# Performance work log

Measured on AMD Instinct MI355X. Metric: run time of the kernel, lower is better.

## Reference

```python
import jax, jax.numpy as jnp
import numpy as np

B, L, S = 4, 512, 100
NG, GS = 19, 5          # 19 clades of 5 species; species 95..99 are singleton clades
VOCAB = 6
HID = 512
HPOOL = 4               # num_attention_heads // 2
D = 64                  # hidden_size / num_attention_heads
ALL = HPOOL * D         # 256
FIRE_H = 32
TIME_SCALE = 1.0        # from time_enc = 'fire_1'
MAX_DIST = 20.0         # config.max_evol_dist


def setup_inputs() -> dict:
    key = jax.random.key(0)
    ks = jax.random.split(key, 10)
    return {
        "source_ids": jax.random.randint(ks[0], (B, L, S), 0, VOCAB, dtype=jnp.int32),
        "in_clade_phylo_dist": jax.random.uniform(ks[1], (S,), dtype=jnp.float32) * MAX_DIST,
        "attn_w_emb": jax.random.normal(ks[2], (VOCAB, HPOOL), dtype=jnp.float32) * 0.02,
        "value_emb": jax.random.normal(ks[3], (VOCAB, ALL), dtype=jnp.float32) * 0.02,
        "ffn_w": jax.random.normal(ks[4], (ALL, HID), dtype=jnp.float32) * 0.02,
        "ffn_b": jnp.zeros((HID,), dtype=jnp.float32),
        "embed_tab": jax.random.normal(ks[5], (VOCAB, HID), dtype=jnp.float32) * 0.02,
        "fire_c": jnp.float32(100.0),
        "fire_w1": jax.random.normal(ks[6], (FIRE_H,), dtype=jnp.float32) * 0.5,
        "fire_w2": jax.random.normal(ks[7], (FIRE_H,), dtype=jnp.float32) * 0.5,
    }


def reference(source_ids, in_clade_phylo_dist, attn_w_emb, value_emb,
              ffn_w, ffn_b, embed_tab, fire_c, fire_w1, fire_w2):
    # --- FIRE time bias: scalar MLP per species distance -> bias[s] ---
    c = jnp.maximum(fire_c, 0.0)
    rel = in_clade_phylo_dist * TIME_SCALE                      # [S]
    rel = jnp.log(c * rel + 1.0) / jnp.log(c * MAX_DIST + 1.0)  # [S]
    h = jax.nn.silu(rel[:, None] * fire_w1[None, :])            # [S, FIRE_H]
    bias = h @ fire_w2                                          # [S]

    # --- multi-species clades: embedding-based attention pooling ---
    grp = jnp.arange(NG * GS).reshape(NG, GS)                   # static clade layout
    ids_g = source_ids[..., :NG * GS].reshape(B, L, NG, GS)     # [B,L,NG,GS]
    scores = jnp.swapaxes(attn_w_emb[ids_g], -1, -2)            # [B,L,NG,H,GS]
    scores = scores + bias[grp][None, None, :, None, :]
    probs = jax.nn.softmax(scores, axis=-1)                     # dropout p=0 (eval)
    vals = value_emb[ids_g].reshape(B, L, NG, GS, HPOOL, D)     # [B,L,NG,GS,H,D]
    pooled = jnp.einsum('blnhg,blnghd->blnhd', probs, vals)     # [B,L,NG,H,D]
    pooled = pooled.reshape(B, L, NG, ALL)
    pooled = pooled @ ffn_w + ffn_b                             # [B,L,NG,HID]

    # --- singleton clades: plain embedding lookup ---
    singles = embed_tab[source_ids[..., NG * GS:]]              # [B,L,5,HID]

    return jnp.concatenate([pooled, singles], axis=-2)          # [B,L,24,HID]
```

## Files before the change

kernel.cpp:

```cpp
#include <hip/hip_runtime.h>

#define B_      4
#define L_      512
#define S_      100
#define NG_     19
#define GS_     5
#define VOCAB_  6
#define HID_    512
#define HPOOL_  4
#define D_      64
#define ALL_    256
#define FIREH_  32
#define MAXDIST_ 20.0f


__global__ __launch_bounds__(128) void prep_kernel(
    const float* __restrict__ dist,
    const float* __restrict__ value_emb,
    const float* __restrict__ ffn_w,
    const float* __restrict__ fire_c,
    const float* __restrict__ fire_w1,
    const float* __restrict__ fire_w2,
    float* __restrict__ bias_out,
    float* __restrict__ W2_out)
{
  const int b = blockIdx.x;
  const int t = threadIdx.x;
  if (b < VOCAB_ * HPOOL_ * 4) {
    const int q   = b >> 2;
    const int col = (b & 3) * 128 + t;
    const int v = q >> 2;
    const int h = q & 3;
    float acc = 0.f;
#pragma unroll
    for (int k = 0; k < D_; ++k) {
      acc = fmaf(value_emb[v * ALL_ + h * D_ + k],
                 ffn_w[(h * D_ + k) * HID_ + col], acc);
    }
    W2_out[q * HID_ + col] = acc;
  } else {
    if (t < S_) {
      const float c = fmaxf(fire_c[0], 0.f);
      const float denom = logf(fmaf(c, MAXDIST_, 1.f));
      const float rel = logf(fmaf(c, dist[t], 1.f)) / denom;
      float acc = 0.f;
#pragma unroll
      for (int i = 0; i < FIREH_; ++i) {
        const float x = rel * fire_w1[i];
        const float s = x / (1.f + expf(-x));
        acc = fmaf(s, fire_w2[i], acc);
      }
      bias_out[t] = acc;
    }
  }
}

__global__ __launch_bounds__(256) void main_kernel(
    const int*   __restrict__ ids,
    const float* __restrict__ attn_w,
    const float* __restrict__ embed_tab,
    const float* __restrict__ ffn_b,
    const float* __restrict__ bias,
    const float* __restrict__ W2,
    float* __restrict__ out)
{
  const int bl = blockIdx.x;
  const int t  = threadIdx.x;

  __shared__ int s_ids[S_];
  __shared__ float s_bias[S_];
  __shared__ float s_aw[VOCAB_ * HPOOL_];
  __shared__ __align__(16) float s_cw[NG_][24];

  if (t < S_) s_ids[t] = ids[bl * S_ + t];
  else if (t >= 100 && t < 200) s_bias[t - 100] = bias[t - 100];
  else if (t >= 224 && t < 248) s_aw[t - 224] = attn_w[t - 224];
#pragma unroll
  for (int i = t; i < NG_ * 24; i += 256) ((float*)s_cw)[i] = 0.f;
  __syncthreads();

  if (t < NG_ * HPOOL_) {
    const int n = t >> 2;
    const int h = t & 3;
    int   idg[GS_];
    float p[GS_];
    float m = -1e30f;
#pragma unroll
    for (int g = 0; g < GS_; ++g) {
      idg[g] = s_ids[n * GS_ + g];
      p[g] = s_aw[idg[g] * HPOOL_ + h] + s_bias[n * GS_ + g];
      m = fmaxf(m, p[g]);
    }
    float s = 0.f;
#pragma unroll
    for (int g = 0; g < GS_; ++g) { p[g] = expf(p[g] - m); s += p[g]; }
    const float inv = 1.f / s;
#pragma unroll
    for (int g = 0; g < GS_; ++g) {
      s_cw[n][idg[g] * HPOOL_ + h] += p[g] * inv;
    }
  }
  __syncthreads();

  float2 w2r[24];
#pragma unroll
  for (int q = 0; q < 24; ++q)
    w2r[q] = *(const float2*)&W2[q * HID_ + 2 * t];
  const float2 bb = *(const float2*)&ffn_b[2 * t];

  float* op = out + (size_t)bl * 24 * HID_ + 2 * t;

  for (int n = 0; n < NG_; ++n) {
    float2 acc = bb;
    const float4* cw4 = (const float4*)s_cw[n];
#pragma unroll
    for (int q4 = 0; q4 < 6; ++q4) {
      const float4 c = cw4[q4];
      acc.x = fmaf(c.x, w2r[q4 * 4 + 0].x, acc.x);
      acc.y = fmaf(c.x, w2r[q4 * 4 + 0].y, acc.y);
      acc.x = fmaf(c.y, w2r[q4 * 4 + 1].x, acc.x);
      acc.y = fmaf(c.y, w2r[q4 * 4 + 1].y, acc.y);
      acc.x = fmaf(c.z, w2r[q4 * 4 + 2].x, acc.x);
      acc.y = fmaf(c.z, w2r[q4 * 4 + 2].y, acc.y);
      acc.x = fmaf(c.w, w2r[q4 * 4 + 3].x, acc.x);
      acc.y = fmaf(c.w, w2r[q4 * 4 + 3].y, acc.y);
    }
    *(float2*)(op + n * HID_) = acc;
  }

#pragma unroll
  for (int j = 0; j < 5; ++j) {
    const int id = s_ids[NG_ * GS_ + j];
    *(float2*)(op + (NG_ + j) * HID_) =
        *(const float2*)&embed_tab[id * HID_ + 2 * t];
  }
}

extern "C" void kernel_launch(void* const* d_in, const int* in_sizes, int n_in,
                              void* d_out, int out_size, void* d_ws, size_t ws_size,
                              hipStream_t stream) {
  const int*   src_ids = (const int*)  d_in[0];
  const float* dist    = (const float*)d_in[1];
  const float* attn_w  = (const float*)d_in[2];
  const float* valemb  = (const float*)d_in[3];
  const float* ffn_w   = (const float*)d_in[4];
  const float* ffn_b   = (const float*)d_in[5];
  const float* emb_tab = (const float*)d_in[6];
  const float* fire_c  = (const float*)d_in[7];
  const float* fire_w1 = (const float*)d_in[8];
  const float* fire_w2 = (const float*)d_in[9];

  float* out  = (float*)d_out;
  float* ws   = (float*)d_ws;
  float* bias = ws;
  float* W2   = ws + 128;

  hipLaunchKernelGGL(prep_kernel, dim3(97), dim3(128), 0, stream,
                     dist, valemb, ffn_w, fire_c, fire_w1, fire_w2, bias, W2);
  hipLaunchKernelGGL(main_kernel, dim3(B_ * L_), dim3(256), 0, stream,
                     src_ids, attn_w, emb_tab, ffn_b, bias, W2, out);
}
```

Baseline: 31.47 us.

## Process two positions per block, hoist W2 loads, use nontemporal stores

Each block now handles two (b,l) positions, which halves the grid and reuses the per-thread W2 register tile and bias across both positions. The W2 loads are moved before the first barrier so they overlap the shared-memory setup. Output writes use nontemporal stores to avoid cache pollution, and the singleton IDs are read directly from global memory. Fewer blocks may reduce parallelism on a large GPU, with 1024 blocks still available.

After: 32.33 us. +2.7%, slower.

```diff
diff --git a/kernel.cpp b/kernel.cpp
--- a/kernel.cpp
+++ b/kernel.cpp
@@ -12,6 +12,9 @@
 #define ALL_    256
 #define FIREH_  32
 #define MAXDIST_ 20.0f
+
+typedef float f32x2 __attribute__((ext_vector_type(2)));
+typedef float f32x4 __attribute__((ext_vector_type(4)));
 
 
 __global__ __launch_bounds__(128) void prep_kernel(
@@ -64,30 +67,40 @@
     const float* __restrict__ W2,
     float* __restrict__ out)
 {
-  const int bl = blockIdx.x;
-  const int t  = threadIdx.x;
+  const int blk = blockIdx.x;
+  const int t   = threadIdx.x;
+  const int bl0 = blk * 2;
 
-  __shared__ int s_ids[S_];
+  __shared__ int   s_ids[2 * S_];
   __shared__ float s_bias[S_];
   __shared__ float s_aw[VOCAB_ * HPOOL_];
-  __shared__ __align__(16) float s_cw[NG_][24];
+  __shared__ __align__(16) float s_cw[2][NG_][24];
 
-  if (t < S_) s_ids[t] = ids[bl * S_ + t];
-  else if (t >= 100 && t < 200) s_bias[t - 100] = bias[t - 100];
-  else if (t >= 224 && t < 248) s_aw[t - 224] = attn_w[t - 224];
+  if (t < 2 * S_) s_ids[t] = ids[bl0 * S_ + t];
+  if (t >= 128 && t < 228) s_bias[t - 128] = bias[t - 128];
+  if (t >= 232) s_aw[t - 232] = attn_w[t - 232];
+
+  f32x2 w2r[24];
 #pragma unroll
-  for (int i = t; i < NG_ * 24; i += 256) ((float*)s_cw)[i] = 0.f;
+  for (int q = 0; q < 24; ++q)
+    w2r[q] = *(const f32x2*)&W2[q * HID_ + 2 * t];
+  const f32x2 bb = *(const f32x2*)&ffn_b[2 * t];
+
+#pragma unroll
+  for (int i = t; i < 2 * NG_ * 24; i += 256) ((float*)s_cw)[i] = 0.f;
   __syncthreads();
 
-  if (t < NG_ * HPOOL_) {
-    const int n = t >> 2;
-    const int h = t & 3;
+  if (t < 2 * NG_ * HPOOL_) {
+    const int r = (t >= 76) ? 1 : 0;
+    const int u = t - 76 * r;
+    const int n = u >> 2;
+    const int h = u & 3;
     int   idg[GS_];
     float p[GS_];
     float m = -1e30f;
 #pragma unroll
     for (int g = 0; g < GS_; ++g) {
-      idg[g] = s_ids[n * GS_ + g];
+      idg[g] = s_ids[r * S_ + n * GS_ + g];
       p[g] = s_aw[idg[g] * HPOOL_ + h] + s_bias[n * GS_ + g];
       m = fmaxf(m, p[g]);
     }
@@ -97,42 +110,39 @@
     const float inv = 1.f / s;
 #pragma unroll
     for (int g = 0; g < GS_; ++g) {
-      s_cw[n][idg[g] * HPOOL_ + h] += p[g] * inv;
+      s_cw[r][n][idg[g] * HPOOL_ + h] += p[g] * inv;
     }
   }
   __syncthreads();
 
-  float2 w2r[24];
 #pragma unroll
-  for (int q = 0; q < 24; ++q)
-    w2r[q] = *(const float2*)&W2[q * HID_ + 2 * t];
-  const float2 bb = *(const float2*)&ffn_b[2 * t];
+  for (int r = 0; r < 2; ++r) {
+    float* op = out + (size_t)(bl0 + r) * 24 * HID_ + 2 * t;
 
-  float* op = out + (size_t)bl * 24 * HID_ + 2 * t;
-
-  for (int n = 0; n < NG_; ++n) {
-    float2 acc = bb;
-    const float4* cw4 = (const float4*)s_cw[n];
+    for (int n = 0; n < NG_; ++n) {
+      f32x2 acc = bb;
+      const f32x4* cw4 = (const f32x4*)s_cw[r][n];
 #pragma unroll
-    for (int q4 = 0; q4 < 6; ++q4) {
-      const float4 c = cw4[q4];
-      acc.x = fmaf(c.x, w2r[q4 * 4 + 0].x, acc.x);
-      acc.y = fmaf(c.x, w2r[q4 * 4 + 0].y, acc.y);
-      acc.x = fmaf(c.y, w2r[q4 * 4 + 1].x, acc.x);
-      acc.y = fmaf(c.y, w2r[q4 * 4 + 1].y, acc.y);
-      acc.x = fmaf(c.z, w2r[q4 * 4 + 2].x, acc.x);
-      acc.y = fmaf(c.z, w2r[q4 * 4 + 2].y, acc.y);
-      acc.x = fmaf(c.w, w2r[q4 * 4 + 3].x, acc.x);
-      acc.y = fmaf(c.w, w2r[q4 * 4 + 3].y, acc.y);
+      for (int q4 = 0; q4 < 6; ++q4) {
+        const f32x4 c = cw4[q4];
+        acc.x = fmaf(c.x, w2r[q4 * 4 + 0].x, acc.x);
+        acc.y = fmaf(c.x, w2r[q4 * 4 + 0].y, acc.y);
+        acc.x = fmaf(c.y, w2r[q4 * 4 + 1].x, acc.x);
+        acc.y = fmaf(c.y, w2r[q4 * 4 + 1].y, acc.y);
+        acc.x = fmaf(c.z, w2r[q4 * 4 + 2].x, acc.x);
+        acc.y = fmaf(c.z, w2r[q4 * 4 + 2].y, acc.y);
+        acc.x = fmaf(c.w, w2r[q4 * 4 + 3].x, acc.x);
+        acc.y = fmaf(c.w, w2r[q4 * 4 + 3].y, acc.y);
+      }
+      __builtin_nontemporal_store(acc, (f32x2*)(op + n * HID_));
     }
-    *(float2*)(op + n * HID_) = acc;
-  }
 
 #pragma unroll
-  for (int j = 0; j < 5; ++j) {
-    const int id = s_ids[NG_ * GS_ + j];
-    *(float2*)(op + (NG_ + j) * HID_) =
-        *(const float2*)&embed_tab[id * HID_ + 2 * t];
+    for (int j = 0; j < 5; ++j) {
+      const int id = ids[(bl0 + r) * S_ + NG_ * GS_ + j];
+      const f32x2 e = *(const f32x2*)&embed_tab[id * HID_ + 2 * t];
+      __builtin_nontemporal_store(e, (f32x2*)(op + (NG_ + j) * HID_));
+    }
   }
 }
 
@@ -157,6 +167,6 @@
 
   hipLaunchKernelGGL(prep_kernel, dim3(97), dim3(128), 0, stream,
                      dist, valemb, ffn_w, fire_c, fire_w1, fire_w2, bias, W2);
-  hipLaunchKernelGGL(main_kernel, dim3(B_ * L_), dim3(256), 0, stream,
+  hipLaunchKernelGGL(main_kernel, dim3(B_ * L_ / 2), dim3(256), 0, stream,
                      src_ids, attn_w, emb_tab, ffn_b, bias, W2, out);
 }
```

## Move per-row softmax clade weights into prep kernel and batch output rows

Applied to the files above, without the earlier changes.

Computes the per-row clade/vocab softmax weight table in the first kernel, alongside the W2 fold and FIRE bias, and stores it in workspace. The output kernel then only loads those weights and streams 2 rows per block, with no shared-memory setup or barriers. The aim is to take the serial softmax phase off the bandwidth-bound write kernel. In exchange it adds a global round trip for the weight table and needs a larger workspace, falling back to the old path when the workspace is too small.

Result: slower. 40.89 us (+29.9%).

```diff
diff --git a/kernel.cpp b/kernel.cpp
--- a/kernel.cpp
+++ b/kernel.cpp
@@ -13,60 +13,184 @@
 #define FIREH_  32
 #define MAXDIST_ 20.0f
 
-
-__global__ __launch_bounds__(128) void prep_kernel(
+typedef float f32x2 __attribute__((ext_vector_type(2)));
+typedef float f32x4 __attribute__((ext_vector_type(4)));
+
+#define CWST_   (NG_ * 24)
+#define NROWS_  (B_ * L_)
+#define WS_W2_   0
+#define WS_CW_   (24 * HID_)
+#define WS_NEED_ ((size_t)(WS_CW_ + NROWS_ * CWST_) * 4)
+
+__global__ __launch_bounds__(256) void k1_kernel(
+    const int*   __restrict__ ids,
     const float* __restrict__ dist,
+    const float* __restrict__ attn_w,
     const float* __restrict__ value_emb,
     const float* __restrict__ ffn_w,
     const float* __restrict__ fire_c,
     const float* __restrict__ fire_w1,
     const float* __restrict__ fire_w2,
-    float* __restrict__ bias_out,
-    float* __restrict__ W2_out)
+    float* __restrict__ W2_out,
+    float* __restrict__ cw_out)
+{
+  const int b = blockIdx.x;
+  const int t = threadIdx.x;
+
+  if (b < 48) {
+    const int q   = b >> 1;
+    const int col = (b & 1) * 256 + t;
+    const int v = q >> 2, h = q & 3;
+    float acc = 0.f;
+#pragma unroll
+    for (int k = 0; k < D_; ++k)
+      acc = fmaf(value_emb[v * ALL_ + h * D_ + k],
+                 ffn_w[(h * D_ + k) * HID_ + col], acc);
+    W2_out[q * HID_ + col] = acc;
+    return;
+  }
+
+  const int cb = b - 48;
+  __shared__ float s_bias[S_];
+  __shared__ float s_aw[VOCAB_ * HPOOL_];
+
+  if (t < S_) {
+    const float c = fmaxf(fire_c[0], 0.f);
+    const float denom = logf(fmaf(c, MAXDIST_, 1.f));
+    const float rel = logf(fmaf(c, dist[t], 1.f)) / denom;
+    float acc = 0.f;
+#pragma unroll
+    for (int i = 0; i < FIREH_; ++i) {
+      const float x = rel * fire_w1[i];
+      acc = fmaf(x / (1.f + expf(-x)), fire_w2[i], acc);
+    }
+    s_bias[t] = acc;
+  } else if (t >= 128 && t < 128 + VOCAB_ * HPOOL_) {
+    s_aw[t - 128] = attn_w[t - 128];
+  }
+  __syncthreads();
+
+  for (int task = t; task < 8 * NG_ * HPOOL_; task += 256) {
+    const int r = task / 76;
+    const int u = task - r * 76;
+    const int n = u >> 2, h = u & 3;
+    const int row = cb * 8 + r;
+
+    int   idg[GS_];
+    float p[GS_];
+    float m = -1e30f;
+#pragma unroll
+    for (int g = 0; g < GS_; ++g) {
+      idg[g] = ids[row * S_ + n * GS_ + g];
+      p[g] = s_aw[idg[g] * HPOOL_ + h] + s_bias[n * GS_ + g];
+      m = fmaxf(m, p[g]);
+    }
+    float s = 0.f;
+#pragma unroll
+    for (int g = 0; g < GS_; ++g) { p[g] = expf(p[g] - m); s += p[g]; }
+    const float inv = 1.f / s;
+
+    float* dst = cw_out + row * CWST_ + n * 24 + h;
+#pragma unroll
+    for (int v = 0; v < VOCAB_; ++v) {
+      float acc = 0.f;
+#pragma unroll
+      for (int g = 0; g < GS_; ++g) acc += (idg[g] == v) ? p[g] : 0.f;
+      dst[v * HPOOL_] = acc * inv;
+    }
+  }
+}
+
+__global__ __launch_bounds__(256) void k2_kernel(
+    const int*   __restrict__ ids,
+    const float* __restrict__ embed_tab,
+    const float* __restrict__ ffn_b,
+    const float* __restrict__ W2,
+    const float* __restrict__ cw,
+    float* __restrict__ out)
+{
+  const int blk = blockIdx.x;
+  const int t   = threadIdx.x;
+  const int bl0 = blk * 2;
+
+  f32x2 w2r[24];
+#pragma unroll
+  for (int q = 0; q < 24; ++q)
+    w2r[q] = *(const f32x2*)&W2[q * HID_ + 2 * t];
+  const f32x2 bb = *(const f32x2*)&ffn_b[2 * t];
+
+#pragma unroll
+  for (int r = 0; r < 2; ++r) {
+    const int row = bl0 + r;
+    const float* __restrict__ cwr = cw + row * CWST_;
+    float* op = out + (size_t)row * 24 * HID_ + 2 * t;
+
+    for (int n = 0; n < NG_; ++n) {
+      f32x2 acc = bb;
+#pragma unroll
+      for (int q4 = 0; q4 < 6; ++q4) {
+        const f32x4 c = *(const f32x4*)&cwr[n * 24 + q4 * 4];
+        acc.x = fmaf(c.x, w2r[q4 * 4 + 0].x, acc.x);
+        acc.y = fmaf(c.x, w2r[q4 * 4 + 0].y, acc.y);
+        acc.x = fmaf(c.y, w2r[q4 * 4 + 1].x, acc.x);
+        acc.y = fmaf(c.y, w2r[q4 * 4 + 1].y, acc.y);
+        acc.x = fmaf(c.z, w2r[q4 * 4 + 2].x, acc.x);
+        acc.y = fmaf(c.z, w2r[q4 * 4 + 2].y, acc.y);
+        acc.x = fmaf(c.w, w2r[q4 * 4 + 3].x, acc.x);
+        acc.y = fmaf(c.w, w2r[q4 * 4 + 3].y, acc.y);
+      }
+      *(f32x2*)(op + n * HID_) = acc;
+    }
+
+#pragma unroll
+    for (int j = 0; j < 5; ++j) {
+      const int id = ids[row * S_ + NG_ * GS_ + j];
+      *(f32x2*)(op + (NG_ + j) * HID_) =
+          *(const f32x2*)&embed_tab[id * HID_ + 2 * t];
+    }
+  }
+}
+
+__global__ __launch_bounds__(128) void prep_kernel(
+    const float* __restrict__ dist, const float* __restrict__ value_emb,
+    const float* __restrict__ ffn_w, const float* __restrict__ fire_c,
+    const float* __restrict__ fire_w1, const float* __restrict__ fire_w2,
+    float* __restrict__ bias_out, float* __restrict__ W2_out)
 {
   const int b = blockIdx.x;
   const int t = threadIdx.x;
   if (b < VOCAB_ * HPOOL_ * 4) {
     const int q   = b >> 2;
     const int col = (b & 3) * 128 + t;
-    const int v = q >> 2;
-    const int h = q & 3;
-    float acc = 0.f;
-#pragma unroll
-    for (int k = 0; k < D_; ++k) {
+    const int v = q >> 2, h = q & 3;
+    float acc = 0.f;
+#pragma unroll
+    for (int k = 0; k < D_; ++k)
       acc = fmaf(value_emb[v * ALL_ + h * D_ + k],
                  ffn_w[(h * D_ + k) * HID_ + col], acc);
-    }
     W2_out[q * HID_ + col] = acc;
-  } else {
-    if (t < S_) {
-      const float c = fmaxf(fire_c[0], 0.f);
-      const float denom = logf(fmaf(c, MAXDIST_, 1.f));
-      const float rel = logf(fmaf(c, dist[t], 1.f)) / denom;
-      float acc = 0.f;
-#pragma unroll
-      for (int i = 0; i < FIREH_; ++i) {
-        const float x = rel * fire_w1[i];
-        const float s = x / (1.f + expf(-x));
-        acc = fmaf(s, fire_w2[i], acc);
-      }
-      bias_out[t] = acc;
-    }
+  } else if (t < S_) {
+    const float c = fmaxf(fire_c[0], 0.f);
+    const float denom = logf(fmaf(c, MAXDIST_, 1.f));
+    const float rel = logf(fmaf(c, dist[t], 1.f)) / denom;
+    float acc = 0.f;
+#pragma unroll
+    for (int i = 0; i < FIREH_; ++i) {
+      const float x = rel * fire_w1[i];
+      acc = fmaf(x / (1.f + expf(-x)), fire_w2[i], acc);
+    }
+    bias_out[t] = acc;
   }
 }
 
 __global__ __launch_bounds__(256) void main_kernel(
-    const int*   __restrict__ ids,
-    const float* __restrict__ attn_w,
-    const float* __restrict__ embed_tab,
-    const float* __restrict__ ffn_b,
-    const float* __restrict__ bias,
-    const float* __restrict__ W2,
+    const int*   __restrict__ ids, const float* __restrict__ attn_w,
+    const float* __restrict__ embed_tab, const float* __restrict__ ffn_b,
+    const float* __restrict__ bias, const float* __restrict__ W2,
     float* __restrict__ out)
 {
   const int bl = blockIdx.x;
   const int t  = threadIdx.x;
-
   __shared__ int s_ids[S_];
   __shared__ float s_bias[S_];
   __shared__ float s_aw[VOCAB_ * HPOOL_];
@@ -80,11 +204,8 @@
   __syncthreads();
 
   if (t < NG_ * HPOOL_) {
-    const int n = t >> 2;
-    const int h = t & 3;
-    int   idg[GS_];
-    float p[GS_];
-    float m = -1e30f;
+    const int n = t >> 2, h = t & 3;
+    int idg[GS_]; float p[GS_]; float m = -1e30f;
 #pragma unroll
     for (int g = 0; g < GS_; ++g) {
       idg[g] = s_ids[n * GS_ + g];
@@ -96,26 +217,24 @@
     for (int g = 0; g < GS_; ++g) { p[g] = expf(p[g] - m); s += p[g]; }
     const float inv = 1.f / s;
 #pragma unroll
-    for (int g = 0; g < GS_; ++g) {
+    for (int g = 0; g < GS_; ++g)
       s_cw[n][idg[g] * HPOOL_ + h] += p[g] * inv;
-    }
   }
   __syncthreads();
 
-  float2 w2r[24];
+  f32x2 w2r[24];
 #pragma unroll
   for (int q = 0; q < 24; ++q)
-    w2r[q] = *(const float2*)&W2[q * HID_ + 2 * t];
-  const float2 bb = *(const float2*)&ffn_b[2 * t];
-
+    w2r[q] = *(const f32x2*)&W2[q * HID_ + 2 * t];
+  const f32x2 bb = *(const f32x2*)&ffn_b[2 * t];
   float* op = out + (size_t)bl * 24 * HID_ + 2 * t;
 
   for (int n = 0; n < NG_; ++n) {
-    float2 acc = bb;
-    const float4* cw4 = (const float4*)s_cw[n];
+    f32x2 acc = bb;
+    const f32x4* cw4 = (const f32x4*)s_cw[n];
 #pragma unroll
     for (int q4 = 0; q4 < 6; ++q4) {
-      const float4 c = cw4[q4];
+      const f32x4 c = cw4[q4];
       acc.x = fmaf(c.x, w2r[q4 * 4 + 0].x, acc.x);
       acc.y = fmaf(c.x, w2r[q4 * 4 + 0].y, acc.y);
       acc.x = fmaf(c.y, w2r[q4 * 4 + 1].x, acc.x);
@@ -125,14 +244,13 @@
       acc.x = fmaf(c.w, w2r[q4 * 4 + 3].x, acc.x);
       acc.y = fmaf(c.w, w2r[q4 * 4 + 3].y, acc.y);
     }
-    *(float2*)(op + n * HID_) = acc;
-  }
-
+    *(f32x2*)(op + n * HID_) = acc;
+  }
 #pragma unroll
   for (int j = 0; j < 5; ++j) {
     const int id = s_ids[NG_ * GS_ + j];
-    *(float2*)(op + (NG_ + j) * HID_) =
-        *(const float2*)&embed_tab[id * HID_ + 2 * t];
+    *(f32x2*)(op + (NG_ + j) * HID_) =
+        *(const f32x2*)&embed_tab[id * HID_ + 2 * t];
   }
 }
 
@@ -150,13 +268,23 @@
   const float* fire_w1 = (const float*)d_in[8];
   const float* fire_w2 = (const float*)d_in[9];
 
-  float* out  = (float*)d_out;
-  float* ws   = (float*)d_ws;
-  float* bias = ws;
-  float* W2   = ws + 128;
-
-  hipLaunchKernelGGL(prep_kernel, dim3(97), dim3(128), 0, stream,
-                     dist, valemb, ffn_w, fire_c, fire_w1, fire_w2, bias, W2);
-  hipLaunchKernelGGL(main_kernel, dim3(B_ * L_), dim3(256), 0, stream,
-                     src_ids, attn_w, emb_tab, ffn_b, bias, W2, out);
-}
+  float* out = (float*)d_out;
+  float* ws  = (float*)d_ws;
+
+  if (ws_size >= WS_NEED_) {
+    float* W2 = ws + WS_W2_;
+    float* cw = ws + WS_CW_;
+    hipLaunchKernelGGL(k1_kernel, dim3(48 + 256), dim3(256), 0, stream,
+                       src_ids, dist, attn_w, valemb, ffn_w,
+                       fire_c, fire_w1, fire_w2, W2, cw);
+    hipLaunchKernelGGL(k2_kernel, dim3(NROWS_ / 2), dim3(256), 0, stream,
+                       src_ids, emb_tab, ffn_b, W2, cw, out);
+  } else {
+    float* bias = ws;
+    float* W2   = ws + 128;
+    hipLaunchKernelGGL(prep_kernel, dim3(97), dim3(128), 0, stream,
+                       dist, valemb, ffn_w, fire_c, fire_w1, fire_w2, bias, W2);
+    hipLaunchKernelGGL(main_kernel, dim3(NROWS_), dim3(256), 0, stream,
+                       src_ids, attn_w, emb_tab, ffn_b, bias, W2, out);
+  }
+}
```
